# Performance work log

Measured on AMD Instinct MI355X. Metric: run time of the kernel, lower is better.

Reference implementation:

```python
import jax, jax.numpy as jnp
import numpy as np

N = 50000      # nodes
E = 800000     # edges (avg degree 16)
D_IN = 16      # raw node feature dim
D = 64         # d_model
H = 8          # heads
DH = D // H    # dim_head = 8
L = 2          # num_encoder_layers
EPS = 1e-5
SCALE = float(np.sqrt(DH))


def _xavier(key, shape):
    fan_in, fan_out = shape[-2], shape[-1]
    a = float(np.sqrt(6.0 / (fan_in + fan_out)))
    return jax.random.uniform(key, shape, jnp.float32, -a, a)


def setup_inputs() -> dict:
    key = jax.random.key(0)
    ks = jax.random.split(key, 20)
    feat = jax.random.normal(ks[0], (N, D_IN), jnp.float32)
    src = jax.random.randint(ks[1], (E,), 0, N, jnp.int32)
    dst = jax.random.randint(ks[2], (E,), 0, N, jnp.int32)
    return {
        "feat": feat,
        "src": src,
        "dst": dst,
        "W_emb": _xavier(ks[3], (D_IN, D)),
        "b_emb": jnp.zeros((D,), jnp.float32),
        "Wq": _xavier(ks[4], (L, D, D)),
        "Wk": _xavier(ks[5], (L, D, D)),
        "Wv": _xavier(ks[6], (L, D, D)),
        "Wo": _xavier(ks[7], (L, D, D)),
        "bo": jnp.zeros((L, D), jnp.float32),
        "bn1_g": jnp.ones((L, D), jnp.float32),
        "bn1_b": jnp.zeros((L, D), jnp.float32),
        "W1": _xavier(ks[8], (L, D, 2 * D)),
        "b1": jnp.zeros((L, 2 * D), jnp.float32),
        "W2": _xavier(ks[9], (L, 2 * D, D)),
        "b2": jnp.zeros((L, D), jnp.float32),
        "bn2_g": jnp.ones((L, D), jnp.float32),
        "bn2_b": jnp.zeros((L, D), jnp.float32),
    }


def _batch_norm(x, g, b):
    # BatchNorm1d (training-mode forward: batch statistics, biased var)
    mu = jnp.mean(x, axis=0)
    var = jnp.var(x, axis=0)
    return (x - mu) / jnp.sqrt(var + EPS) * g + b


def _layer(h, src, dst, Wq, Wk, Wv, Wo, bo, bn1_g, bn1_b, W1, b1, W2, b2, bn2_g, bn2_b):
    h_in1 = h
    Q = (h @ Wq).reshape(N, H, DH)
    K = (h @ Wk).reshape(N, H, DH)
    V = (h @ Wv).reshape(N, H, DH)
    # SDDMM: per-edge dot(K[src], Q[dst]) -> [E, H]
    e = jnp.sum(K[src] * Q[dst], axis=-1)
    # scaled_exp: exp(clamp(score/sqrt(dh), -10, 10)) stored as edge 'score'
    e = jnp.exp(jnp.clip(e / SCALE, -10.0, 10.0))
    # reduce_func then applies a softmax over mailbox scores (double exp, faithful)
    m = jax.ops.segment_max(e, dst, num_segments=N)          # [N, H]
    w = jnp.exp(e - m[dst])                                   # [E, H]
    s = jax.ops.segment_sum(w, dst, num_segments=N)           # [N, H]
    alpha = w / s[dst]                                        # [E, H]
    out = jax.ops.segment_sum(alpha[:, :, None] * V[src], dst, num_segments=N)
    h = out.reshape(N, D) @ Wo + bo
    h = _batch_norm(h_in1 + h, bn1_g, bn1_b)
    h_in2 = h
    h = jax.nn.relu(h @ W1 + b1) @ W2 + b2
    h = _batch_norm(h + h_in2, bn2_g, bn2_b)
    return h


def reference(feat, src, dst, W_emb, b_emb, Wq, Wk, Wv, Wo, bo, bn1_g, bn1_b,
              W1, b1, W2, b2, bn2_g, bn2_b):
    h = feat @ W_emb + b_emb  # embedding_h (dropout=0)
    for l in range(L):
        h = _layer(h, src, dst, Wq[l], Wk[l], Wv[l], Wo[l], bo[l],
                   bn1_g[l], bn1_b[l], W1[l], b1[l], W2[l], b2[l],
                   bn2_g[l], bn2_b[l])
    return h
```

## Files before the change

kernel.cpp:

```cpp
#include <hip/hip_runtime.h>

#define NNODES 50000
#define NEDGES 800000
#define DM 64
#define NH 8
#define DH 8
#define EPSN 1e-5f
#define INV_SCALE 0.3535533905932738f
#define SCAN_BLOCKS 200
#define SCAN_CHUNK  250

template<int KA, int KB, int R, bool RELU, bool RES, bool STATS>
__global__ __launch_bounds__(256, 2) void gemm_k(const float* __restrict__ A,
    const float* __restrict__ W, int woff,
    const float* __restrict__ bias, int boff,
    float* __restrict__ C, float* __restrict__ stats, int Nrows)
{
    constexpr int CG   = KB / 4;
    constexpr int RG   = 256 / CG;
    constexpr int ROWS = RG * R;
    constexpr int APAD = KA + 4;
    constexpr int KAq  = KA / 4;

    __shared__ __align__(16) float sW[KA * KB];
    __shared__ __align__(16) float sA[ROWS * APAD];

    const int tid  = threadIdx.x;
    const int row0 = blockIdx.x * ROWS;

    for (int i4 = tid; i4 < KA * KB / 4; i4 += 256)
        *(float4*)&sW[i4 * 4] = ((const float4*)(W + woff))[i4];
    for (int i4 = tid; i4 < ROWS * KAq; i4 += 256) {
        int r = i4 / KAq, kq = i4 - r * KAq;
        int gr = row0 + r;
        float4 v = make_float4(0.f, 0.f, 0.f, 0.f);
        if (gr < Nrows) v = ((const float4*)A)[(size_t)gr * KAq + kq];
        *(float4*)&sA[r * APAD + kq * 4] = v;
    }
    __syncthreads();

    const int cg = tid % CG, rg = tid / CG;
    const int c0 = cg * 4, r0 = rg * R;

    float4 acc[R];
#pragma unroll
    for (int rr = 0; rr < R; rr++) acc[rr] = make_float4(0.f, 0.f, 0.f, 0.f);

#pragma unroll 2
    for (int k = 0; k < KA; k += 4) {
        float4 w0 = *(const float4*)&sW[(k + 0) * KB + c0];
        float4 w1 = *(const float4*)&sW[(k + 1) * KB + c0];
        float4 w2 = *(const float4*)&sW[(k + 2) * KB + c0];
        float4 w3 = *(const float4*)&sW[(k + 3) * KB + c0];
#pragma unroll
        for (int rr = 0; rr < R; rr++) {
            float4 av = *(const float4*)&sA[(r0 + rr) * APAD + k];
            acc[rr].x += av.x * w0.x + av.y * w1.x + av.z * w2.x + av.w * w3.x;
            acc[rr].y += av.x * w0.y + av.y * w1.y + av.z * w2.y + av.w * w3.y;
            acc[rr].z += av.x * w0.z + av.y * w1.z + av.z * w2.z + av.w * w3.z;
            acc[rr].w += av.x * w0.w + av.y * w1.w + av.z * w2.w + av.w * w3.w;
        }
    }

    float4 bv = make_float4(0.f, 0.f, 0.f, 0.f);
    if (bias) {
        bv.x = bias[boff + c0];     bv.y = bias[boff + c0 + 1];
        bv.z = bias[boff + c0 + 2]; bv.w = bias[boff + c0 + 3];
    }

    float4 vals[R];
#pragma unroll
    for (int rr = 0; rr < R; rr++) {
        int grow = row0 + r0 + rr;
        bool valid = grow < Nrows;
        float4 v;
        v.x = acc[rr].x + bv.x; v.y = acc[rr].y + bv.y;
        v.z = acc[rr].z + bv.z; v.w = acc[rr].w + bv.w;
        if (RELU) {
            v.x = fmaxf(v.x, 0.f); v.y = fmaxf(v.y, 0.f);
            v.z = fmaxf(v.z, 0.f); v.w = fmaxf(v.w, 0.f);
        }
        if (valid) {
            if (RES) {
                float4 old = *(const float4*)&C[(size_t)grow * KB + c0];
                v.x += old.x; v.y += old.y; v.z += old.z; v.w += old.w;
            }
            *(float4*)&C[(size_t)grow * KB + c0] = v;
        } else {
            v = make_float4(0.f, 0.f, 0.f, 0.f);
        }
        vals[rr] = v;
    }

    if (STATS) {
        __syncthreads();
        float4 cs = make_float4(0.f, 0.f, 0.f, 0.f);
#pragma unroll
        for (int rr = 0; rr < R; rr++) {
            cs.x += vals[rr].x; cs.y += vals[rr].y;
            cs.z += vals[rr].z; cs.w += vals[rr].w;
        }
        *(float4*)&sA[rg * KB + c0] = cs;
        __syncthreads();
        if (tid < KB) {
            float s = 0.f;
#pragma unroll
            for (int g = 0; g < RG; g++) s += sA[g * KB + tid];
            atomicAdd(&stats[tid], s);
        }
        __syncthreads();
        float4 cq = make_float4(0.f, 0.f, 0.f, 0.f);
#pragma unroll
        for (int rr = 0; rr < R; rr++) {
            cq.x += vals[rr].x * vals[rr].x; cq.y += vals[rr].y * vals[rr].y;
            cq.z += vals[rr].z * vals[rr].z; cq.w += vals[rr].w * vals[rr].w;
        }
        *(float4*)&sA[rg * KB + c0] = cq;
        __syncthreads();
        if (tid < KB) {
            float s = 0.f;
#pragma unroll
            for (int g = 0; g < RG; g++) s += sA[g * KB + tid];
            atomicAdd(&stats[KB + tid], s);
        }
    }
}

__global__ __launch_bounds__(256, 2) void qkv_k(const float* __restrict__ A,
    const float* __restrict__ Wq, const float* __restrict__ Wk,
    const float* __restrict__ Wv, int woff,
    float* __restrict__ Qo, float* __restrict__ Ko, float* __restrict__ Vo,
    int Nrows)
{
    constexpr int APAD = 68;
    __shared__ __align__(16) float sW[64 * 64];
    __shared__ __align__(16) float sA[64 * APAD];

    const int tid  = threadIdx.x;
    const int row0 = blockIdx.x * 64;

    for (int i4 = tid; i4 < 64 * 16; i4 += 256) {
        int r = i4 >> 4, kq = i4 & 15;
        int gr = row0 + r;
        float4 v = make_float4(0.f, 0.f, 0.f, 0.f);
        if (gr < Nrows) v = ((const float4*)A)[(size_t)gr * 16 + kq];
        *(float4*)&sA[r * APAD + kq * 4] = v;
    }

    const float* Ws[3]   = {Wq, Wk, Wv};
    float*       Outs[3] = {Qo, Ko, Vo};

    const int cg = tid & 15, rg = tid >> 4;
    const int c0 = cg * 4, r0 = rg * 4;

    for (int m = 0; m < 3; m++) {
        __syncthreads();
        for (int i4 = tid; i4 < 1024; i4 += 256)
            *(float4*)&sW[i4 * 4] = ((const float4*)(Ws[m] + woff))[i4];
        __syncthreads();

        float4 acc[4];
#pragma unroll
        for (int rr = 0; rr < 4; rr++) acc[rr] = make_float4(0.f, 0.f, 0.f, 0.f);

#pragma unroll 2
        for (int k = 0; k < 64; k += 4) {
            float4 w0 = *(const float4*)&sW[(k + 0) * 64 + c0];
            float4 w1 = *(const float4*)&sW[(k + 1) * 64 + c0];
            float4 w2 = *(const float4*)&sW[(k + 2) * 64 + c0];
            float4 w3 = *(const float4*)&sW[(k + 3) * 64 + c0];
#pragma unroll
            for (int rr = 0; rr < 4; rr++) {
                float4 av = *(const float4*)&sA[(r0 + rr) * APAD + k];
                acc[rr].x += av.x * w0.x + av.y * w1.x + av.z * w2.x + av.w * w3.x;
                acc[rr].y += av.x * w0.y + av.y * w1.y + av.z * w2.y + av.w * w3.y;
                acc[rr].z += av.x * w0.z + av.y * w1.z + av.z * w2.z + av.w * w3.z;
                acc[rr].w += av.x * w0.w + av.y * w1.w + av.z * w2.w + av.w * w3.w;
            }
        }

#pragma unroll
        for (int rr = 0; rr < 4; rr++) {
            int grow = row0 + r0 + rr;
            if (grow < Nrows)
                *(float4*)&Outs[m][(size_t)grow * 64 + c0] = acc[rr];
        }
    }
}

__global__ __launch_bounds__(256) void bn_apply(const float* __restrict__ Hin,
    float* __restrict__ Hout, const float* __restrict__ stats,
    const float* __restrict__ g, int goff, const float* __restrict__ b, int boff)
{
    int i = blockIdx.x * 256 + threadIdx.x;
    if (i >= NNODES * DM) return;
    int c = i & 63;
    float mu  = stats[c] * (1.0f / NNODES);
    float var = stats[64 + c] * (1.0f / NNODES) - mu * mu;
    float istd = rsqrtf(fmaxf(var, 0.0f) + EPSN);
    Hout[i] = (Hin[i] - mu) * istd * g[goff + c] + b[boff + c];
}

__global__ __launch_bounds__(256) void zero_int_k(int* __restrict__ p, int n)
{
    int i = blockIdx.x * 256 + threadIdx.x;
    if (i < n) p[i] = 0;
}

__global__ __launch_bounds__(256) void count_k(const int* __restrict__ dst,
                                               int* __restrict__ cursor)
{
    int e = blockIdx.x * 256 + threadIdx.x;
    if (e < NEDGES) atomicAdd(&cursor[dst[e]], 1);
}

__global__ __launch_bounds__(256) void csr_scanA(const int* __restrict__ cursor,
                                                 int* __restrict__ bsum)
{
    __shared__ int red[256];
    const int base = blockIdx.x * SCAN_CHUNK;
    int s = 0;
    for (int i = threadIdx.x; i < SCAN_CHUNK; i += 256) s += cursor[base + i];
    red[threadIdx.x] = s;
    __syncthreads();
    for (int o = 128; o > 0; o >>= 1) {
        if (threadIdx.x < o) red[threadIdx.x] += red[threadIdx.x + o];
        __syncthreads();
    }
    if (threadIdx.x == 0) bsum[blockIdx.x] = red[0];
}

__global__ __launch_bounds__(256) void csr_scanB(int* __restrict__ bsum)
{
    __shared__ int t[256];
    const int tid = threadIdx.x;
    int v = (tid < SCAN_BLOCKS) ? bsum[tid] : 0;
    t[tid] = v;
    __syncthreads();
    for (int off = 1; off < 256; off <<= 1) {
        int x = (tid >= off) ? t[tid - off] : 0;
        __syncthreads();
        t[tid] += x;
        __syncthreads();
    }
    if (tid < SCAN_BLOCKS) bsum[tid] = t[tid] - v;
}

__global__ __launch_bounds__(256) void csr_scanC(int* __restrict__ cursor,
    int* __restrict__ rowptr, const int* __restrict__ bsum)
{
    __shared__ int t[256];
    const int base = blockIdx.x * SCAN_CHUNK;
    const int tid  = threadIdx.x;
    int deg = (tid < SCAN_CHUNK) ? cursor[base + tid] : 0;
    t[tid] = deg;
    __syncthreads();
    for (int off = 1; off < 256; off <<= 1) {
        int x = (tid >= off) ? t[tid - off] : 0;
        __syncthreads();
        t[tid] += x;
        __syncthreads();
    }
    int excl = bsum[blockIdx.x] + t[tid] - deg;
    if (tid < SCAN_CHUNK) {
        rowptr[base + tid] = excl;
        cursor[base + tid] = excl;
    }
    if (blockIdx.x == 0 && tid == 0) rowptr[NNODES] = NEDGES;
}

__global__ __launch_bounds__(256) void fill_k(const int* __restrict__ src,
    const int* __restrict__ dst, int* __restrict__ cursor,
    int* __restrict__ nbr)
{
    int e = blockIdx.x * 256 + threadIdx.x;
    if (e >= NEDGES) return;
    int pos = atomicAdd(&cursor[dst[e]], 1);
    nbr[pos] = src[e];
}

__global__ __launch_bounds__(256) void attn_fused_k(const float* __restrict__ Q,
    const float* __restrict__ K, const float* __restrict__ V,
    const int* __restrict__ rowptr, const int* __restrict__ nbr,
    float* __restrict__ U)
{
    const int w = threadIdx.x >> 6;
    const int d = blockIdx.x * 4 + w;
    if (d >= NNODES) return;
    const int l  = threadIdx.x & 63;
    const int el = l >> 3;
    const int h  = l & 7;
    const int e0 = rowptr[d], e1 = rowptr[d + 1];
    const int deg = e1 - e0;

    if (deg == 0) {
        U[(size_t)d * DM + h * DH + el] = 0.f;
        return;
    }

    const float4* qp = (const float4*)(Q + (size_t)d * DM + h * DH);
    const float4 q0 = qp[0], q1 = qp[1];

    float m = 0.0f;
    float S = 0.0f;
    float u[8] = {0.f, 0.f, 0.f, 0.f, 0.f, 0.f, 0.f, 0.f};

    for (int base = 0; base < deg; base += 16) {
        const int i0 = base + el, i1 = base + 8 + el;
        const bool v0ok = i0 < deg, v1ok = i1 < deg;
        const int s0 = nbr[e0 + (v0ok ? i0 : 0)];
        const int s1 = nbr[e0 + (v1ok ? i1 : 0)];

        const float4* kp0 = (const float4*)(K + (size_t)s0 * DM + h * DH);
        const float4* vp0 = (const float4*)(V + (size_t)s0 * DM + h * DH);
        const float4* kp1 = (const float4*)(K + (size_t)s1 * DM + h * DH);
        const float4* vp1 = (const float4*)(V + (size_t)s1 * DM + h * DH);
        float4 ka0 = kp0[0], ka1 = kp0[1];
        float4 kb0 = kp1[0], kb1 = kp1[1];
        float4 va0 = vp0[0], va1 = vp0[1];
        float4 vb0 = vp1[0], vb1 = vp1[1];

        float d0 = ka0.x * q0.x + ka0.y * q0.y + ka0.z * q0.z + ka0.w * q0.w
                 + ka1.x * q1.x + ka1.y * q1.y + ka1.z * q1.z + ka1.w * q1.w;
        float d1 = kb0.x * q0.x + kb0.y * q0.y + kb0.z * q0.z + kb0.w * q0.w
                 + kb1.x * q1.x + kb1.y * q1.y + kb1.z * q1.z + kb1.w * q1.w;

        float ev0 = __expf(fminf(fmaxf(d0 * INV_SCALE, -10.f), 10.f));
        float ev1 = __expf(fminf(fmaxf(d1 * INV_SCALE, -10.f), 10.f));
        if (!v0ok) ev0 = 0.f;
        if (!v1ok) ev1 = 0.f;

        float bm = fmaxf(ev0, ev1);
        bm = fmaxf(bm, __shfl_xor(bm, 8, 64));
        bm = fmaxf(bm, __shfl_xor(bm, 16, 64));
        bm = fmaxf(bm, __shfl_xor(bm, 32, 64));

        const float mn = fmaxf(m, bm);
        const float r  = __expf(m - mn);
        const float w0 = v0ok ? __expf(ev0 - mn) : 0.f;
        const float w1 = v1ok ? __expf(ev1 - mn) : 0.f;

        S = S * r + w0 + w1;
        u[0] = u[0] * r + w0 * va0.x + w1 * vb0.x;
        u[1] = u[1] * r + w0 * va0.y + w1 * vb0.y;
        u[2] = u[2] * r + w0 * va0.z + w1 * vb0.z;
        u[3] = u[3] * r + w0 * va0.w + w1 * vb0.w;
        u[4] = u[4] * r + w0 * va1.x + w1 * vb1.x;
        u[5] = u[5] * r + w0 * va1.y + w1 * vb1.y;
        u[6] = u[6] * r + w0 * va1.z + w1 * vb1.z;
        u[7] = u[7] * r + w0 * va1.w + w1 * vb1.w;
        m = mn;
    }

#pragma unroll
    for (int off = 8; off <= 32; off <<= 1) {
        S += __shfl_xor(S, off, 64);
#pragma unroll
        for (int j = 0; j < 8; j++) u[j] += __shfl_xor(u[j], off, 64);
    }

    const float out = (S > 0.f) ? u[el] / S : 0.f;
    U[(size_t)d * DM + h * DH + el] = out;
}

__global__ __launch_bounds__(256) void fill_const_k(float* __restrict__ out, int n)
{
    int i = blockIdx.x * 256 + threadIdx.x;
    if (i < n) out[i] = 100.0f;
}

extern "C" void kernel_launch(void* const* d_in, const int* in_sizes, int n_in,
                              void* d_out, int out_size, void* d_ws, size_t ws_size,
                              hipStream_t stream)
{
    const int expect[18] = {800000, 800000, 800000, 1024, 64,
                            8192, 8192, 8192, 8192, 128,
                            128, 128, 16384, 256, 16384, 128, 128, 128};
    bool order_ok = (n_in == 18) && (out_size == NNODES * DM);
    if (order_ok)
        for (int i = 0; i < 18; i++)
            if (in_sizes[i] != expect[i]) { order_ok = false; break; }
    if (!order_ok) {
        fill_const_k<<<(out_size + 255) / 256, 256, 0, stream>>>((float*)d_out,
                                                                 out_size);
        return;
    }

    const float* feat  = (const float*)d_in[0];
    const int*   src   = (const int*)d_in[1];
    const int*   dst   = (const int*)d_in[2];
    const float* W_emb = (const float*)d_in[3];
    const float* b_emb = (const float*)d_in[4];
    const float* Wq    = (const float*)d_in[5];
    const float* Wk    = (const float*)d_in[6];
    const float* Wv    = (const float*)d_in[7];
    const float* Wo    = (const float*)d_in[8];
    const float* bo    = (const float*)d_in[9];
    const float* bn1_g = (const float*)d_in[10];
    const float* bn1_b = (const float*)d_in[11];
    const float* W1    = (const float*)d_in[12];
    const float* b1    = (const float*)d_in[13];
    const float* W2    = (const float*)d_in[14];
    const float* b2    = (const float*)d_in[15];
    const float* bn2_g = (const float*)d_in[16];
    const float* bn2_b = (const float*)d_in[17];

    const size_t ND = (size_t)NNODES * DM;
    float* ws     = (float*)d_ws;
    float* Hb     = ws;
    float* Qb     = Hb + ND;
    float* Kb     = Qb + ND;
    float* Vb     = Kb + ND;
    float* Ub     = Vb + ND;
    float* stats  = Ub + ND;
    int*   rowptr = (int*)(stats + 256);
    int*   cursor = rowptr + (NNODES + 1);
    int*   bsum   = cursor + NNODES;
    int*   nbr    = bsum + SCAN_BLOCKS;
    float* Fb     = Qb;

    const size_t BASE = (5 * ND + 256) * 4
                      + ((NNODES + 1) + NNODES + SCAN_BLOCKS + NEDGES) * 4;
    if (ws_size < BASE) {
        fill_const_k<<<(out_size + 255) / 256, 256, 0, stream>>>((float*)d_out,
                                                                 out_size);
        return;
    }

    const int g64 = (NNODES + 63) / 64;
    const int g32 = (NNODES + 31) / 32;
    const int gND = (int)(ND / 256);
    const int gE  = (NEDGES + 255) / 256;
    const int gAT = (NNODES + 3) / 4;

    zero_int_k<<<(NNODES + 255) / 256, 256, 0, stream>>>(cursor, NNODES);
    count_k<<<gE, 256, 0, stream>>>(dst, cursor);
    csr_scanA<<<SCAN_BLOCKS, 256, 0, stream>>>(cursor, bsum);
    csr_scanB<<<1, 256, 0, stream>>>(bsum);
    csr_scanC<<<SCAN_BLOCKS, 256, 0, stream>>>(cursor, rowptr, bsum);
    fill_k<<<gE, 256, 0, stream>>>(src, dst, cursor, nbr);

    gemm_k<16, 64, 4, false, false, false>
        <<<g64, 256, 0, stream>>>(feat, W_emb, 0, b_emb, 0, Hb, nullptr, NNODES);

    for (int l = 0; l < 2; l++) {
        const int woff  = l * DM * DM;
        const int w1off = l * DM * 2 * DM;
        const int boff  = l * DM;
        const int b1off = l * 2 * DM;

        qkv_k<<<g64, 256, 0, stream>>>(Hb, Wq, Wk, Wv, woff, Qb, Kb, Vb, NNODES);

        attn_fused_k<<<gAT, 256, 0, stream>>>(Qb, Kb, Vb, rowptr, nbr, Ub);

        hipMemsetAsync(stats, 0, 128 * 4, stream);
        gemm_k<64, 64, 4, false, true, true>
            <<<g64, 256, 0, stream>>>(Ub, Wo, woff, bo, boff, Hb, stats, NNODES);
        bn_apply<<<gND, 256, 0, stream>>>(Hb, Hb, stats, bn1_g, boff, bn1_b, boff);

        gemm_k<64, 128, 4, true, false, false>
            <<<g32, 256, 0, stream>>>(Hb, W1, w1off, b1, b1off, Fb, nullptr, NNODES);
        hipMemsetAsync(stats, 0, 128 * 4, stream);
        gemm_k<128, 64, 2, false, true, true>
            <<<g32, 256, 0, stream>>>(Fb, W2, w1off, b2, boff, Hb, stats, NNODES);
        float* outp = (l == 1) ? (float*)d_out : Hb;
        bn_apply<<<gND, 256, 0, stream>>>(Hb, outp, stats, bn2_g, boff, bn2_b, boff);
    }
}
```

Baseline: 605.1 us.

## Fuse BatchNorm application into consumers and merge FFN GEMMs into one kernel

```diff
diff --git a/kernel.cpp b/kernel.cpp
--- a/kernel.cpp
+++ b/kernel.cpp
@@ -10,11 +10,13 @@
 #define SCAN_BLOCKS 200
 #define SCAN_CHUNK  250
 
-template<int KA, int KB, int R, bool RELU, bool RES, bool STATS>
+template<int KA, int KB, int R, bool RELU, bool RES, bool STATS, bool BNRES>
 __global__ __launch_bounds__(256, 2) void gemm_k(const float* __restrict__ A,
     const float* __restrict__ W, int woff,
     const float* __restrict__ bias, int boff,
-    float* __restrict__ C, float* __restrict__ stats, int Nrows)
+    float* __restrict__ C, float* __restrict__ stats,
+    const float* __restrict__ bnstats, const float* __restrict__ bng, int bgoff,
+    const float* __restrict__ bnb, int bboff, int Nrows)
 {
     constexpr int CG   = KB / 4;
     constexpr int RG   = 256 / CG;
@@ -66,6 +68,21 @@
     if (bias) {
         bv.x = bias[boff + c0];     bv.y = bias[boff + c0 + 1];
         bv.z = bias[boff + c0 + 2]; bv.w = bias[boff + c0 + 3];
+    }
+
+    float4 scR = make_float4(1.f, 1.f, 1.f, 1.f);
+    float4 ofR = make_float4(0.f, 0.f, 0.f, 0.f);
+    if (BNRES) {
+        const float inv_n = 1.0f / NNODES;
+#pragma unroll
+        for (int j = 0; j < 4; j++) {
+            float mu   = bnstats[c0 + j] * inv_n;
+            float var  = bnstats[KB + c0 + j] * inv_n - mu * mu;
+            float istd = rsqrtf(fmaxf(var, 0.f) + EPSN);
+            float s    = istd * bng[bgoff + c0 + j];
+            ((float*)&scR)[j] = s;
+            ((float*)&ofR)[j] = bnb[bboff + c0 + j] - mu * s;
+        }
     }
 
     float4 vals[R];
@@ -83,6 +100,12 @@
         if (valid) {
             if (RES) {
                 float4 old = *(const float4*)&C[(size_t)grow * KB + c0];
+                if (BNRES) {
+                    old.x = old.x * scR.x + ofR.x;
+                    old.y = old.y * scR.y + ofR.y;
+                    old.z = old.z * scR.z + ofR.z;
+                    old.w = old.w * scR.w + ofR.w;
+                }
                 v.x += old.x; v.y += old.y; v.z += old.z; v.w += old.w;
             }
             *(float4*)&C[(size_t)grow * KB + c0] = v;
@@ -126,11 +149,13 @@
     }
 }
 
+template<bool BNIN>
 __global__ __launch_bounds__(256, 2) void qkv_k(const float* __restrict__ A,
     const float* __restrict__ Wq, const float* __restrict__ Wk,
     const float* __restrict__ Wv, int woff,
     float* __restrict__ Qo, float* __restrict__ Ko, float* __restrict__ Vo,
-    int Nrows)
+    const float* __restrict__ bnstats, const float* __restrict__ bng, int bgoff,
+    const float* __restrict__ bnb, int bboff, int Nrows)
 {
     constexpr int APAD = 68;
     __shared__ __align__(16) float sW[64 * 64];
@@ -139,12 +164,35 @@
     const int tid  = threadIdx.x;
     const int row0 = blockIdx.x * 64;
 
-    for (int i4 = tid; i4 < 64 * 16; i4 += 256) {
-        int r = i4 >> 4, kq = i4 & 15;
-        int gr = row0 + r;
-        float4 v = make_float4(0.f, 0.f, 0.f, 0.f);
-        if (gr < Nrows) v = ((const float4*)A)[(size_t)gr * 16 + kq];
-        *(float4*)&sA[r * APAD + kq * 4] = v;
+    {
+        const int kq = tid & 15, cc = kq * 4;
+        float4 sc = make_float4(1.f, 1.f, 1.f, 1.f);
+        float4 of = make_float4(0.f, 0.f, 0.f, 0.f);
+        if (BNIN) {
+            const float inv_n = 1.0f / NNODES;
+#pragma unroll
+            for (int j = 0; j < 4; j++) {
+                float mu   = bnstats[cc + j] * inv_n;
+                float var  = bnstats[64 + cc + j] * inv_n - mu * mu;
+                float istd = rsqrtf(fmaxf(var, 0.f) + EPSN);
+                float s    = istd * bng[bgoff + cc + j];
+                ((float*)&sc)[j] = s;
+                ((float*)&of)[j] = bnb[bboff + cc + j] - mu * s;
+            }
+        }
+        for (int i4 = tid; i4 < 64 * 16; i4 += 256) {
+            int r = i4 >> 4;
+            int gr = row0 + r;
+            float4 v = make_float4(0.f, 0.f, 0.f, 0.f);
+            if (gr < Nrows) {
+                v = ((const float4*)A)[(size_t)gr * 16 + kq];
+                if (BNIN) {
+                    v.x = v.x * sc.x + of.x; v.y = v.y * sc.y + of.y;
+                    v.z = v.z * sc.z + of.z; v.w = v.w * sc.w + of.w;
+                }
+            }
+            *(float4*)&sA[r * APAD + cc] = v;
+        }
     }
 
     const float* Ws[3]   = {Wq, Wk, Wv};
@@ -185,6 +233,165 @@
             if (grow < Nrows)
                 *(float4*)&Outs[m][(size_t)grow * 64 + c0] = acc[rr];
         }
+    }
+}
+
+__global__ __launch_bounds__(256, 2) void ffn_k(float* __restrict__ H,
+    const float* __restrict__ W1, int w1off,
+    const float* __restrict__ b1, int b1off,
+    const float* __restrict__ W2, int w2off,
+    const float* __restrict__ b2, int b2off,
+    const float* __restrict__ bnstats,
+    const float* __restrict__ bng, int bgoff,
+    const float* __restrict__ bnb, int bboff,
+    float* __restrict__ stats2, int Nrows)
+{
+    constexpr int APAD = 68, FPAD = 132;
+    __shared__ __align__(16) float sW[128 * 64];
+    __shared__ __align__(16) float sA[32 * APAD];
+    __shared__ __align__(16) float sF[32 * FPAD];
+
+    const int tid  = threadIdx.x;
+    const int row0 = blockIdx.x * 32;
+
+    for (int i4 = tid; i4 < 2048; i4 += 256)
+        *(float4*)&sW[i4 * 4] = ((const float4*)(W1 + w1off))[i4];
+
+    {
+        const int kq = tid & 15, cc = kq * 4;
+        const float inv_n = 1.0f / NNODES;
+        float4 sc, of;
+#pragma unroll
+        for (int j = 0; j < 4; j++) {
+            float mu   = bnstats[cc + j] * inv_n;
+            float var  = bnstats[64 + cc + j] * inv_n - mu * mu;
+            float istd = rsqrtf(fmaxf(var, 0.f) + EPSN);
+            float s    = istd * bng[bgoff + cc + j];
+            ((float*)&sc)[j] = s;
+            ((float*)&of)[j] = bnb[bboff + cc + j] - mu * s;
+        }
+        for (int i4 = tid; i4 < 512; i4 += 256) {
+            int r = i4 >> 4;
+            int gr = row0 + r;
+            float4 v = make_float4(0.f, 0.f, 0.f, 0.f);
+            if (gr < Nrows) {
+                v = ((const float4*)H)[(size_t)gr * 16 + kq];
+                v.x = v.x * sc.x + of.x; v.y = v.y * sc.y + of.y;
+                v.z = v.z * sc.z + of.z; v.w = v.w * sc.w + of.w;
+            }
+            *(float4*)&sA[r * APAD + cc] = v;
+        }
+    }
+    __syncthreads();
+
+    {
+        const int cg = tid & 31, rg = tid >> 5;
+        const int c0 = cg * 4, r0 = rg * 4;
+        float4 acc[4];
+#pragma unroll
+        for (int rr = 0; rr < 4; rr++) acc[rr] = make_float4(0.f, 0.f, 0.f, 0.f);
+#pragma unroll 2
+        for (int k = 0; k < 64; k += 4) {
+            float4 w0 = *(const float4*)&sW[(k + 0) * 128 + c0];
+            float4 w1 = *(const float4*)&sW[(k + 1) * 128 + c0];
+            float4 w2 = *(const float4*)&sW[(k + 2) * 128 + c0];
+            float4 w3 = *(const float4*)&sW[(k + 3) * 128 + c0];
+#pragma unroll
+            for (int rr = 0; rr < 4; rr++) {
+                float4 av = *(const float4*)&sA[(r0 + rr) * APAD + k];
+                acc[rr].x += av.x * w0.x + av.y * w1.x + av.z * w2.x + av.w * w3.x;
+                acc[rr].y += av.x * w0.y + av.y * w1.y + av.z * w2.y + av.w * w3.y;
+                acc[rr].z += av.x * w0.z + av.y * w1.z + av.z * w2.z + av.w * w3.z;
+                acc[rr].w += av.x * w0.w + av.y * w1.w + av.z * w2.w + av.w * w3.w;
+            }
+        }
+        float4 bb;
+        bb.x = b1[b1off + c0];     bb.y = b1[b1off + c0 + 1];
+        bb.z = b1[b1off + c0 + 2]; bb.w = b1[b1off + c0 + 3];
+#pragma unroll
+        for (int rr = 0; rr < 4; rr++) {
+            float4 v;
+            v.x = fmaxf(acc[rr].x + bb.x, 0.f);
+            v.y = fmaxf(acc[rr].y + bb.y, 0.f);
+            v.z = fmaxf(acc[rr].z + bb.z, 0.f);
+            v.w = fmaxf(acc[rr].w + bb.w, 0.f);
+            *(float4*)&sF[(r0 + rr) * FPAD + c0] = v;
+        }
+    }
+    __syncthreads();
+
+    for (int i4 = tid; i4 < 2048; i4 += 256)
+        *(float4*)&sW[i4 * 4] = ((const float4*)(W2 + w2off))[i4];
+    __syncthreads();
+
+    const int cg = tid & 15, rg = tid >> 4;
+    const int c0 = cg * 4, r0 = rg * 2;
+    float4 acc[2];
+#pragma unroll
+    for (int rr = 0; rr < 2; rr++) acc[rr] = make_float4(0.f, 0.f, 0.f, 0.f);
+#pragma unroll 2
+    for (int k = 0; k < 128; k += 4) {
+        float4 w0 = *(const float4*)&sW[(k + 0) * 64 + c0];
+        float4 w1 = *(const float4*)&sW[(k + 1) * 64 + c0];
+        float4 w2 = *(const float4*)&sW[(k + 2) * 64 + c0];
+        float4 w3 = *(const float4*)&sW[(k + 3) * 64 + c0];
+#pragma unroll
+        for (int rr = 0; rr < 2; rr++) {
+            float4 fv = *(const float4*)&sF[(r0 + rr) * FPAD + k];
+            acc[rr].x += fv.x * w0.x + fv.y * w1.x + fv.z * w2.x + fv.w * w3.x;
+            acc[rr].y += fv.x * w0.y + fv.y * w1.y + fv.z * w2.y + fv.w * w3.y;
+            acc[rr].z += fv.x * w0.z + fv.y * w1.z + fv.z * w2.z + fv.w * w3.z;
+            acc[rr].w += fv.x * w0.w + fv.y * w1.w + fv.z * w2.w + fv.w * w3.w;
+        }
+    }
+    float4 bb;
+    bb.x = b2[b2off + c0];     bb.y = b2[b2off + c0 + 1];
+    bb.z = b2[b2off + c0 + 2]; bb.w = b2[b2off + c0 + 3];
+
+    float4 vals[2];
+#pragma unroll
+    for (int rr = 0; rr < 2; rr++) {
+        int grow = row0 + r0 + rr;
+        bool valid = grow < Nrows;
+        float4 res = *(const float4*)&sA[(r0 + rr) * APAD + c0];
+        float4 v;
+        v.x = acc[rr].x + bb.x + res.x;
+        v.y = acc[rr].y + bb.y + res.y;
+        v.z = acc[rr].z + bb.z + res.z;
+        v.w = acc[rr].w + bb.w + res.w;
+        if (valid) {
+            *(float4*)&H[(size_t)grow * 64 + c0] = v;
+        } else {
+            v = make_float4(0.f, 0.f, 0.f, 0.f);
+        }
+        vals[rr] = v;
+    }
+
+    __syncthreads();
+    float4 cs;
+    cs.x = vals[0].x + vals[1].x; cs.y = vals[0].y + vals[1].y;
+    cs.z = vals[0].z + vals[1].z; cs.w = vals[0].w + vals[1].w;
+    *(float4*)&sA[rg * 64 + c0] = cs;
+    __syncthreads();
+    if (tid < 64) {
+        float s = 0.f;
+#pragma unroll
+        for (int g = 0; g < 16; g++) s += sA[g * 64 + tid];
+        atomicAdd(&stats2[tid], s);
+    }
+    __syncthreads();
+    float4 cq;
+    cq.x = vals[0].x * vals[0].x + vals[1].x * vals[1].x;
+    cq.y = vals[0].y * vals[0].y + vals[1].y * vals[1].y;
+    cq.z = vals[0].z * vals[0].z + vals[1].z * vals[1].z;
+    cq.w = vals[0].w * vals[0].w + vals[1].w * vals[1].w;
+    *(float4*)&sA[rg * 64 + c0] = cq;
+    __syncthreads();
+    if (tid < 64) {
+        float s = 0.f;
+#pragma unroll
+        for (int g = 0; g < 16; g++) s += sA[g * 64 + tid];
+        atomicAdd(&stats2[64 + tid], s);
     }
 }
 
@@ -417,7 +624,9 @@
     int*   cursor = rowptr + (NNODES + 1);
     int*   bsum   = cursor + NNODES;
     int*   nbr    = bsum + SCAN_BLOCKS;
-    float* Fb     = Qb;
+
+    float* statsA = stats;
+    float* statsB = stats + 128;
 
     const size_t BASE = (5 * ND + 256) * 4
                       + ((NNODES + 1) + NNODES + SCAN_BLOCKS + NEDGES) * 4;
@@ -440,30 +649,43 @@
     csr_scanC<<<SCAN_BLOCKS, 256, 0, stream>>>(cursor, rowptr, bsum);
     fill_k<<<gE, 256, 0, stream>>>(src, dst, cursor, nbr);
 
-    gemm_k<16, 64, 4, false, false, false>
-        <<<g64, 256, 0, stream>>>(feat, W_emb, 0, b_emb, 0, Hb, nullptr, NNODES);
+    gemm_k<16, 64, 4, false, false, false, false>
+        <<<g64, 256, 0, stream>>>(feat, W_emb, 0, b_emb, 0, Hb, nullptr,
+                                  nullptr, nullptr, 0, nullptr, 0, NNODES);
 
     for (int l = 0; l < 2; l++) {
         const int woff  = l * DM * DM;
         const int w1off = l * DM * 2 * DM;
         const int boff  = l * DM;
         const int b1off = l * 2 * DM;
-
-        qkv_k<<<g64, 256, 0, stream>>>(Hb, Wq, Wk, Wv, woff, Qb, Kb, Vb, NNODES);
+        const int poff  = (l - 1) * DM;
+
+        if (l == 0)
+            qkv_k<false><<<g64, 256, 0, stream>>>(Hb, Wq, Wk, Wv, woff,
+                Qb, Kb, Vb, nullptr, nullptr, 0, nullptr, 0, NNODES);
+        else
+            qkv_k<true><<<g64, 256, 0, stream>>>(Hb, Wq, Wk, Wv, woff,
+                Qb, Kb, Vb, statsB, bn2_g, poff, bn2_b, poff, NNODES);
 
         attn_fused_k<<<gAT, 256, 0, stream>>>(Qb, Kb, Vb, rowptr, nbr, Ub);
 
-        hipMemsetAsync(stats, 0, 128 * 4, stream);
-        gemm_k<64, 64, 4, false, true, true>
-            <<<g64, 256, 0, stream>>>(Ub, Wo, woff, bo, boff, Hb, stats, NNODES);
-        bn_apply<<<gND, 256, 0, stream>>>(Hb, Hb, stats, bn1_g, boff, bn1_b, boff);
-
-        gemm_k<64, 128, 4, true, false, false>
-            <<<g32, 256, 0, stream>>>(Hb, W1, w1off, b1, b1off, Fb, nullptr, NNODES);
-        hipMemsetAsync(stats, 0, 128 * 4, stream);
-        gemm_k<128, 64, 2, false, true, true>
-            <<<g32, 256, 0, stream>>>(Fb, W2, w1off, b2, boff, Hb, stats, NNODES);
-        float* outp = (l == 1) ? (float*)d_out : Hb;
-        bn_apply<<<gND, 256, 0, stream>>>(Hb, outp, stats, bn2_g, boff, bn2_b, boff);
-    }
-}
+        hipMemsetAsync(statsA, 0, 128 * 4, stream);
+        if (l == 0)
+            gemm_k<64, 64, 4, false, true, true, false>
+                <<<g64, 256, 0, stream>>>(Ub, Wo, woff, bo, boff, Hb, statsA,
+                                          nullptr, nullptr, 0, nullptr, 0, NNODES);
+        else
+            gemm_k<64, 64, 4, false, true, true, true>
+                <<<g64, 256, 0, stream>>>(Ub, Wo, woff, bo, boff, Hb, statsA,
+                                          statsB, bn2_g, poff, bn2_b, poff, NNODES);
+
+        hipMemsetAsync(statsB, 0, 128 * 4, stream);
+        ffn_k<<<g32, 256, 0, stream>>>(Hb, W1, w1off, b1, b1off,
+                                       W2, w1off, b2, boff,
+                                       statsA, bn1_g, boff, bn1_b, boff,
+                                       statsB, NNODES);
+    }
+
+    bn_apply<<<gND, 256, 0, stream>>>(Hb, (float*)d_out, statsB,
+                                      bn2_g, DM, bn2_b, DM);
+}
```

Measured after the change: 556.0 us. -8.1%, faster.
